# Kernel tuning notes

Measured on AMD Instinct MI355X. Metric: run time of the kernel, lower is better.

The kernel has to match this reference:

```python
import jax, jax.numpy as jnp
import numpy as np

EMBED_DIM = 1024
NUM_HEADS = 16
HEAD_DIM = EMBED_DIM // NUM_HEADS


def setup_inputs() -> dict:
    key = jax.random.key(0)
    ks = jax.random.split(key, 9)
    B, T, C = 2, 2048, EMBED_DIM
    s = 1.0 / np.sqrt(C)
    inp = {
        "x": jax.random.normal(ks[0], (B, T, C), dtype=jnp.float32),
        "Wq": jax.random.uniform(ks[1], (C, C), jnp.float32, -s, s),
        "bq": jax.random.uniform(ks[2], (C,), jnp.float32, -s, s),
        "Wk": jax.random.uniform(ks[3], (C, C), jnp.float32, -s, s),
        "bk": jax.random.uniform(ks[4], (C,), jnp.float32, -s, s),
        "Wv": jax.random.uniform(ks[5], (C, C), jnp.float32, -s, s),
        "bv": jax.random.uniform(ks[6], (C,), jnp.float32, -s, s),
        "Wo": jax.random.uniform(ks[7], (C, C), jnp.float32, -s, s),
        "bo": jax.random.uniform(ks[8], (C,), jnp.float32, -s, s),
    }
    return inp


def reference(x, Wq, bq, Wk, bk, Wv, bv, Wo, bo):
    B, T, C = x.shape
    H, D = NUM_HEADS, HEAD_DIM

    def heads(W, b):
        # [B,T,C] -> [B,H,T,D]
        return (x @ W + b).reshape(B, T, H, D).transpose(0, 2, 1, 3)

    q = heads(Wq, bq)
    k = heads(Wk, bk)
    v = heads(Wv, bv)

    scores = jnp.einsum('bhtd,bhsd->bhts', q, k) / np.sqrt(D).astype(np.float32)
    causal = jnp.tril(jnp.ones((T, T), dtype=bool))  # [T,T]
    scores = jnp.where(causal[None, None], scores, -jnp.inf)
    weights = jax.nn.softmax(scores, axis=-1)
    out = jnp.einsum('bhts,bhsd->bhtd', weights, v)  # [B,H,T,D]
    out = out.transpose(0, 2, 1, 3).reshape(B, T, C)
    return out @ Wo + bo
```

## Files before the change

### kernel.cpp

```cpp
#include <hip/hip_runtime.h>
#include <stdint.h>

#define T_LEN 2048
#define C_DIM 1024
#define NHEAD 16
#define HDIM  64
#define MTOT  4096

typedef __bf16 bf16;
typedef __bf16 bf16x8 __attribute__((ext_vector_type(8)));
typedef float  f32x4  __attribute__((ext_vector_type(4)));

__device__ __forceinline__ bf16 f2bf(float f) {
    union { float f; unsigned u; } x; x.f = f;
    unsigned r = x.u + 0x7fffu + ((x.u >> 16) & 1u);
    unsigned short h = (unsigned short)(r >> 16);
    return __builtin_bit_cast(bf16, h);
}

__device__ __forceinline__ void g2l16(const void* g, const void* l) {
    __builtin_amdgcn_global_load_lds(
        (const __attribute__((address_space(1))) unsigned int*)(uintptr_t)g,
        (__attribute__((address_space(3))) unsigned int*)(uint32_t)(uintptr_t)l,
        16, 0, 0);
}


__global__ void cast_x_kernel(const float* __restrict__ x, bf16* __restrict__ xb) {
    int f = blockIdx.x * 256 + threadIdx.x;
    const float4* p = (const float4*)x + (size_t)f * 2;
    float4 a = p[0], b = p[1];
    bf16x8 o;
    o[0] = f2bf(a.x); o[1] = f2bf(a.y); o[2] = f2bf(a.z); o[3] = f2bf(a.w);
    o[4] = f2bf(b.x); o[5] = f2bf(b.y); o[6] = f2bf(b.z); o[7] = f2bf(b.w);
    ((bf16x8*)xb)[f] = o;
}

__global__ void cast_w_kernel(const float* __restrict__ W0, const float* __restrict__ W1,
                              const float* __restrict__ W2, const float* __restrict__ W3,
                              bf16* __restrict__ wt) {
    __shared__ float tile[64][68];
    const int tid = threadIdx.x;
    const int w = blockIdx.z;
    const float* W = (w == 0) ? W0 : (w == 1) ? W1 : (w == 2) ? W2 : W3;
    const int kb = blockIdx.x * 64, nb = blockIdx.y * 64;
#pragma unroll
    for (int pass = 0; pass < 4; ++pass) {
        int row = pass * 16 + (tid >> 4);
        int col = (tid & 15) * 4;
        float4 v = *(const float4*)(W + (size_t)(kb + row) * 1024 + nb + col);
        *(float4*)(&tile[row][col]) = v;
    }
    __syncthreads();
#pragma unroll
    for (int pass = 0; pass < 2; ++pass) {
        int s = pass * 256 + tid;
        int nn = s >> 3, c = s & 7;
        bf16x8 o;
#pragma unroll
        for (int j = 0; j < 8; ++j) o[j] = f2bf(tile[c * 8 + j][nn]);
        *(bf16x8*)(wt + (size_t)w * 1048576 + (size_t)(nb + nn) * 1024 + kb + c * 8) = o;
    }
}

__global__ void transpose_v_kernel(const bf16* __restrict__ V, bf16* __restrict__ Vtp) {
    __shared__ bf16 tile[128][72];
    const int tid = threadIdx.x;
    const int t0 = blockIdx.x * 128, bh = blockIdx.y;
    const size_t hb = (size_t)bh * 131072;
#pragma unroll
    for (int pass = 0; pass < 4; ++pass) {
        int s = pass * 256 + tid;
        int row = s >> 3, c = s & 7;
        bf16x8 v = *(const bf16x8*)(V + hb + (size_t)(t0 + row) * 64 + c * 8);
        *(bf16x8*)(&tile[row][c * 8]) = v;
    }
    __syncthreads();
#pragma unroll
    for (int pass = 0; pass < 4; ++pass) {
        int s = pass * 256 + tid;
        int d = s >> 4, ch = s & 15;
        bf16x8 o;
#pragma unroll
        for (int j = 0; j < 8; ++j) o[j] = tile[j * 16 + ch][d];
        *(bf16x8*)(Vtp + hb + (size_t)d * 2048 + t0 + ch * 8) = o;
    }
}

__global__ __launch_bounds__(256, 3)
void gemm_bt_kernel(const bf16* __restrict__ A, const bf16* __restrict__ WtAll,
                    const float* __restrict__ b0, const float* __restrict__ b1,
                    const float* __restrict__ b2, bf16* __restrict__ outQKV) {
    __shared__ char lds[32768];
    bf16* As = (bf16*)lds;
    bf16* Bs = (bf16*)(lds + 16384);

    const int tid = threadIdx.x;
    const int lane = tid & 63, wid = tid >> 6;
    const int r = lane & 15, q4 = lane >> 4;
    const int mbase = blockIdx.y * 128;
    const int nbase = blockIdx.x * 128;
    const int z = blockIdx.z;
    const bf16* Bt = WtAll + (size_t)z * 1048576;
    const float* bias = (z == 0) ? b0 : (z == 1) ? b1 : b2;
    const float osc = (z == 0) ? 0.125f : 1.0f;

    const int wm = (wid >> 1) * 64;
    const int wn = (wid & 1) * 64;

    float bv[4];
#pragma unroll
    for (int j = 0; j < 4; ++j) bv[j] = bias[nbase + wn + j * 16 + r];

    f32x4 acc[4][4];
#pragma unroll
    for (int i = 0; i < 4; ++i)
#pragma unroll
        for (int j = 0; j < 4; ++j) acc[i][j] = f32x4{0.f, 0.f, 0.f, 0.f};

    for (int kt = 0; kt < 16; ++kt) {
        int kb = kt * 64;
#pragma unroll
        for (int p = 0; p < 4; ++p) {
            int s = p * 256 + tid;
            int row = s >> 3, blk = s & 7;
            int sb = blk ^ (row & 7);
            g2l16(A  + (size_t)(mbase + row) * 1024 + kb + sb * 8, (char*)As + s * 16);
            g2l16(Bt + (size_t)(nbase + row) * 1024 + kb + sb * 8, (char*)Bs + s * 16);
        }
        __syncthreads();
#pragma unroll
        for (int ks = 0; ks < 2; ++ks) {
            int blk = ks * 4 + q4;
            bf16x8 a[4], b[4];
#pragma unroll
            for (int i = 0; i < 4; ++i) {
                int rowa = wm + i * 16 + r;
                a[i] = *(const bf16x8*)((const char*)As + rowa * 128 + ((blk ^ (rowa & 7)) * 16));
                int rowb = wn + i * 16 + r;
                b[i] = *(const bf16x8*)((const char*)Bs + rowb * 128 + ((blk ^ (rowb & 7)) * 16));
            }
#pragma unroll
            for (int i = 0; i < 4; ++i)
#pragma unroll
                for (int j = 0; j < 4; ++j)
                    acc[i][j] = __builtin_amdgcn_mfma_f32_16x16x32_bf16(a[i], b[j], acc[i][j], 0, 0, 0);
        }
        __syncthreads();
    }

#pragma unroll
    for (int i = 0; i < 4; ++i) {
        int m0 = mbase + wm + i * 16 + q4 * 4;
#pragma unroll
        for (int j = 0; j < 4; ++j) {
            int n = nbase + wn + j * 16 + r;
#pragma unroll
            for (int reg = 0; reg < 4; ++reg) {
                float v = (acc[i][j][reg] + bv[j]) * osc;
                int mm = m0 + reg;
                int bi = mm >> 11, t = mm & 2047, h = n >> 6, d = n & 63;
                outQKV[(size_t)z * 4194304 + ((size_t)(bi * 16 + h) * 2048 + t) * 64 + d] = f2bf(v);
            }
        }
    }
}

__global__ __launch_bounds__(256, 2)
void gemm_o_kernel(const bf16* __restrict__ A, const bf16* __restrict__ Bt,
                   const float* __restrict__ bias, float* __restrict__ out) {
    __shared__ char lds[24576];
    bf16* As = (bf16*)lds;
    bf16* Bs = (bf16*)(lds + 16384);

    const int tid = threadIdx.x;
    const int lane = tid & 63, wid = tid >> 6;
    const int r = lane & 15, q4 = lane >> 4;
    const int nb = blockIdx.x * 64;
    const int mb = blockIdx.y * 128;
    const int wm = (wid >> 1) * 64;
    const int wn = (wid & 1) * 32;

    float bv[2];
#pragma unroll
    for (int j = 0; j < 2; ++j) bv[j] = bias[nb + wn + j * 16 + r];

    f32x4 acc[4][2];
#pragma unroll
    for (int i = 0; i < 4; ++i)
#pragma unroll
        for (int j = 0; j < 2; ++j) acc[i][j] = f32x4{0.f, 0.f, 0.f, 0.f};

    for (int kt = 0; kt < 16; ++kt) {
        int kb = kt * 64;
#pragma unroll
        for (int p = 0; p < 4; ++p) {
            int s = p * 256 + tid;
            int row = s >> 3, blk = s & 7;
            g2l16(A + (size_t)(mb + row) * 1024 + kb + ((blk ^ (row & 7)) * 8), (char*)As + s * 16);
        }
#pragma unroll
        for (int p = 0; p < 2; ++p) {
            int s = p * 256 + tid;
            int row = s >> 3, blk = s & 7;
            g2l16(Bt + (size_t)(nb + row) * 1024 + kb + ((blk ^ (row & 7)) * 8), (char*)Bs + s * 16);
        }
        __syncthreads();
#pragma unroll
        for (int ks = 0; ks < 2; ++ks) {
            int blk = ks * 4 + q4;
            bf16x8 a[4], b[2];
#pragma unroll
            for (int i = 0; i < 4; ++i) {
                int rowa = wm + i * 16 + r;
                a[i] = *(const bf16x8*)((const char*)As + rowa * 128 + ((blk ^ (rowa & 7)) * 16));
            }
#pragma unroll
            for (int j = 0; j < 2; ++j) {
                int rowb = wn + j * 16 + r;
                b[j] = *(const bf16x8*)((const char*)Bs + rowb * 128 + ((blk ^ (rowb & 7)) * 16));
            }
#pragma unroll
            for (int i = 0; i < 4; ++i)
#pragma unroll
                for (int j = 0; j < 2; ++j)
                    acc[i][j] = __builtin_amdgcn_mfma_f32_16x16x32_bf16(a[i], b[j], acc[i][j], 0, 0, 0);
        }
        __syncthreads();
    }

#pragma unroll
    for (int i = 0; i < 4; ++i) {
        int m0 = mb + wm + i * 16 + q4 * 4;
#pragma unroll
        for (int j = 0; j < 2; ++j) {
            int n = nb + wn + j * 16 + r;
#pragma unroll
            for (int reg = 0; reg < 4; ++reg)
                out[(size_t)(m0 + reg) * 1024 + n] = acc[i][j][reg] + bv[j];
        }
    }
}

__global__ __launch_bounds__(256, 1)
void attn_kernel(const bf16* __restrict__ Q, const bf16* __restrict__ K,
                 const bf16* __restrict__ Vtp, bf16* __restrict__ Aout) {
    __shared__ char lds[98304];

    const int tid = threadIdx.x, lane = tid & 63, wid = tid >> 6;
    const int r = lane & 15, q4 = lane >> 4;
    const int p = blockIdx.x >> 5;
    const int bh = blockIdx.x & 31;
    const int b = bh >> 4, h = bh & 15;
    const size_t hb = (size_t)bh * 131072;
    char* Pw = lds + 65536 + wid * 8192;

    const int qiA = p, qiB = 15 - p;
    const int itB0 = qiA + 1;
    const int ittot = itB0 + qiB + 1;

    bf16x8 qfA[2][2], qfB[2][2], qf[2][2];
#pragma unroll
    for (int i = 0; i < 2; ++i)
#pragma unroll
        for (int ks = 0; ks < 2; ++ks) {
            int rA = qiA * 128 + wid * 32 + i * 16 + r;
            int rB = qiB * 128 + wid * 32 + i * 16 + r;
            qfA[i][ks] = *(const bf16x8*)(Q + hb + (size_t)rA * 64 + ks * 32 + q4 * 8);
            qfB[i][ks] = *(const bf16x8*)(Q + hb + (size_t)rB * 64 + ks * 32 + q4 * 8);
            qf[i][ks] = qfA[i][ks];
        }

    f32x4 o[2][4];
    float lip[2][4];
#pragma unroll
    for (int i = 0; i < 2; ++i)
#pragma unroll
        for (int jd = 0; jd < 4; ++jd) { o[i][jd] = f32x4{0.f, 0.f, 0.f, 0.f}; lip[i][jd] = 0.f; }

    auto stage = [&](int buf, int kb) {
        char* Kb = lds + buf * 16384;
        char* Vb = lds + 32768 + buf * 16384;
#pragma unroll
        for (int pp = 0; pp < 4; ++pp) {
            int s = pp * 256 + tid;
            int row = s >> 3, blk = s & 7;
            g2l16(K + hb + (size_t)(kb + row) * 64 + ((blk ^ (row & 7)) * 8), Kb + s * 16);
        }
#pragma unroll
        for (int pp = 0; pp < 4; ++pp) {
            int s = pp * 256 + tid;
            int row = s >> 4, ch = s & 15;
            g2l16(Vtp + hb + (size_t)row * 2048 + kb + ((ch ^ (row & 15)) * 8), Vb + s * 16);
        }
    };

    auto epilogue = [&](int qbase) {
#pragma unroll
        for (int i = 0; i < 2; ++i)
#pragma unroll
            for (int reg = 0; reg < 4; ++reg) {
                float li = lip[i][reg];
                li += __shfl_xor(li, 1);
                li += __shfl_xor(li, 2);
                li += __shfl_xor(li, 4);
                li += __shfl_xor(li, 8);
                float inv = 1.f / li;
                int grow = qbase + wid * 32 + i * 16 + q4 * 4 + reg;
#pragma unroll
                for (int jd = 0; jd < 4; ++jd) {
                    int d = jd * 16 + r;
                    Aout[((size_t)(b * 2048 + grow)) * 1024 + h * 64 + d] = f2bf(o[i][jd][reg] * inv);
                }
            }
    };

    stage(0, 0);

    for (int it = 0; it < ittot; ++it) {
        __syncthreads();
        const int cb = it & 1;
        if (it + 1 < ittot) {
            int nit = it + 1;
            int nkt = (nit < itB0) ? nit : (nit - itB0);
            stage(nit & 1, nkt * 128);
        }
        if (it == itB0) {
            epilogue(qiA * 128);
#pragma unroll
            for (int i = 0; i < 2; ++i) {
#pragma unroll
                for (int jd = 0; jd < 4; ++jd) { o[i][jd] = f32x4{0.f, 0.f, 0.f, 0.f}; lip[i][jd] = 0.f; }
#pragma unroll
                for (int ks = 0; ks < 2; ++ks) qf[i][ks] = qfB[i][ks];
            }
        }
        const bool inB = (it >= itB0);
        const int qi = inB ? qiB : qiA;
        const int kt = inB ? (it - itB0) : it;
        const int kb = kt * 128;
        const int qbase = qi * 128;
        const char* Kb = lds + cb * 16384;
        const char* Vb = lds + 32768 + cb * 16384;

        f32x4 sc[2][8];
#pragma unroll
        for (int jn = 0; jn < 8; ++jn) {
            int rowk = jn * 16 + r;
            bf16x8 bk0 = *(const bf16x8*)(Kb + rowk * 128 + ((q4 ^ (rowk & 7)) * 16));
            bf16x8 bk1 = *(const bf16x8*)(Kb + rowk * 128 + (((4 + q4) ^ (rowk & 7)) * 16));
#pragma unroll
            for (int i = 0; i < 2; ++i) {
                sc[i][jn] = __builtin_amdgcn_mfma_f32_16x16x32_bf16(qf[i][0], bk0, f32x4{0.f, 0.f, 0.f, 0.f}, 0, 0, 0);
                sc[i][jn] = __builtin_amdgcn_mfma_f32_16x16x32_bf16(qf[i][1], bk1, sc[i][jn], 0, 0, 0);
            }
        }

        const bool lastt = (kt == qi);
#pragma unroll
        for (int i = 0; i < 2; ++i) {
#pragma unroll
            for (int reg = 0; reg < 4; ++reg) {
                int rowl = i * 16 + q4 * 4 + reg;
                int grow = qbase + wid * 32 + rowl;
                bf16x8 pp8;
                float rs = 0.f;
                if (lastt) {
#pragma unroll
                    for (int jn = 0; jn < 8; ++jn) {
                        float sv = (kb + jn * 16 + r > grow) ? -1e30f : sc[i][jn][reg];
                        float pv = __expf(sv);
                        rs += pv;
                        pp8[jn] = (bf16)pv;
                    }
                } else {
#pragma unroll
                    for (int jn = 0; jn < 8; ++jn) {
                        float pv = __expf(sc[i][jn][reg]);
                        rs += pv;
                        pp8[jn] = (bf16)pv;
                    }
                }
                lip[i][reg] += rs;
                *(bf16x8*)(Pw + rowl * 256 + ((r ^ (rowl & 15)) * 16)) = pp8;
            }
        }

#pragma unroll
        for (int s4 = 0; s4 < 4; ++s4) {
            int c = s4 * 4 + q4;
            bf16x8 ap0 = *(const bf16x8*)(Pw + r * 256 + ((c ^ r) * 16));
            bf16x8 ap1 = *(const bf16x8*)(Pw + (16 + r) * 256 + ((c ^ r) * 16));
#pragma unroll
            for (int jd = 0; jd < 4; ++jd) {
                int rowd = jd * 16 + r;
                bf16x8 bv8 = *(const bf16x8*)(Vb + rowd * 256 + ((c ^ (rowd & 15)) * 16));
                o[0][jd] = __builtin_amdgcn_mfma_f32_16x16x32_bf16(ap0, bv8, o[0][jd], 0, 0, 0);
                o[1][jd] = __builtin_amdgcn_mfma_f32_16x16x32_bf16(ap1, bv8, o[1][jd], 0, 0, 0);
            }
        }
    }

    epilogue(qiB * 128);
}


extern "C" void kernel_launch(void* const* d_in, const int* in_sizes, int n_in,
                              void* d_out, int out_size, void* d_ws, size_t ws_size,
                              hipStream_t stream) {
    const float* x  = (const float*)d_in[0];
    const float* Wq = (const float*)d_in[1];
    const float* bq = (const float*)d_in[2];
    const float* Wk = (const float*)d_in[3];
    const float* bk = (const float*)d_in[4];
    const float* Wv = (const float*)d_in[5];
    const float* bv = (const float*)d_in[6];
    const float* Wo = (const float*)d_in[7];
    const float* bo = (const float*)d_in[8];
    float* out = (float*)d_out;

    char* ws = (char*)d_ws;
    bf16* xb   = (bf16*)(ws);
    bf16* wt   = (bf16*)(ws + 8388608);
    bf16* qkv  = (bf16*)(ws + 16777216);
    bf16* vtp  = (bf16*)(ws + 41943040);
    bf16* attn = (bf16*)(ws + 50331648);

    hipLaunchKernelGGL(cast_x_kernel, dim3(2048), dim3(256), 0, stream, x, xb);
    hipLaunchKernelGGL(cast_w_kernel, dim3(16, 16, 4), dim3(256), 0, stream, Wq, Wk, Wv, Wo, wt);
    hipLaunchKernelGGL(gemm_bt_kernel, dim3(8, 32, 3), dim3(256), 0, stream,
                       xb, wt, bq, bk, bv, qkv);
    hipLaunchKernelGGL(transpose_v_kernel, dim3(16, 32), dim3(256), 0, stream,
                       qkv + (size_t)2 * 4194304, vtp);
    hipLaunchKernelGGL(attn_kernel, dim3(256), dim3(256), 0, stream,
                       qkv, qkv + 4194304, vtp, attn);
    hipLaunchKernelGGL(gemm_o_kernel, dim3(16, 32), dim3(256), 0, stream,
                       attn, wt + (size_t)3 * 1048576, bo, out);
}
```

Measured before the change: 184.9 us.

## Keep attention probabilities in registers via transposed MFMA and permuted V layout

```diff
diff --git a/kernel.cpp b/kernel.cpp
--- a/kernel.cpp
+++ b/kernel.cpp
@@ -8,6 +8,7 @@
 #define MTOT  4096
 
 typedef __bf16 bf16;
+typedef __bf16 bf16x4 __attribute__((ext_vector_type(4)));
 typedef __bf16 bf16x8 __attribute__((ext_vector_type(8)));
 typedef float  f32x4  __attribute__((ext_vector_type(4)));
 
@@ -82,12 +83,15 @@
         int d = s >> 4, ch = s & 15;
         bf16x8 o;
 #pragma unroll
-        for (int j = 0; j < 8; ++j) o[j] = tile[j * 16 + ch][d];
+        for (int j = 0; j < 8; ++j) {
+            int orig = 32 * (ch >> 2) + 16 * (j >> 2) + 4 * (ch & 3) + (j & 3);
+            o[j] = tile[orig][d];
+        }
         *(bf16x8*)(Vtp + hb + (size_t)d * 2048 + t0 + ch * 8) = o;
     }
 }
 
-__global__ __launch_bounds__(256, 3)
+__global__ __launch_bounds__(256, 2)
 void gemm_bt_kernel(const bf16* __restrict__ A, const bf16* __restrict__ WtAll,
                     const float* __restrict__ b0, const float* __restrict__ b1,
                     const float* __restrict__ b2, bf16* __restrict__ outQKV) {
@@ -245,7 +249,7 @@
 __global__ __launch_bounds__(256, 1)
 void attn_kernel(const bf16* __restrict__ Q, const bf16* __restrict__ K,
                  const bf16* __restrict__ Vtp, bf16* __restrict__ Aout) {
-    __shared__ char lds[98304];
+    __shared__ char lds[65536];
 
     const int tid = threadIdx.x, lane = tid & 63, wid = tid >> 6;
     const int r = lane & 15, q4 = lane >> 4;
@@ -253,30 +257,30 @@
     const int bh = blockIdx.x & 31;
     const int b = bh >> 4, h = bh & 15;
     const size_t hb = (size_t)bh * 131072;
-    char* Pw = lds + 65536 + wid * 8192;
 
     const int qiA = p, qiB = 15 - p;
     const int itB0 = qiA + 1;
     const int ittot = itB0 + qiB + 1;
 
-    bf16x8 qfA[2][2], qfB[2][2], qf[2][2];
+    bf16x8 qf[2][2], qfB[2][2];
 #pragma unroll
     for (int i = 0; i < 2; ++i)
 #pragma unroll
         for (int ks = 0; ks < 2; ++ks) {
             int rA = qiA * 128 + wid * 32 + i * 16 + r;
             int rB = qiB * 128 + wid * 32 + i * 16 + r;
-            qfA[i][ks] = *(const bf16x8*)(Q + hb + (size_t)rA * 64 + ks * 32 + q4 * 8);
+            qf[i][ks]  = *(const bf16x8*)(Q + hb + (size_t)rA * 64 + ks * 32 + q4 * 8);
             qfB[i][ks] = *(const bf16x8*)(Q + hb + (size_t)rB * 64 + ks * 32 + q4 * 8);
-            qf[i][ks] = qfA[i][ks];
         }
 
     f32x4 o[2][4];
-    float lip[2][4];
-#pragma unroll
-    for (int i = 0; i < 2; ++i)
-#pragma unroll
-        for (int jd = 0; jd < 4; ++jd) { o[i][jd] = f32x4{0.f, 0.f, 0.f, 0.f}; lip[i][jd] = 0.f; }
+    float lip[2];
+#pragma unroll
+    for (int i = 0; i < 2; ++i) {
+        lip[i] = 0.f;
+#pragma unroll
+        for (int jd = 0; jd < 4; ++jd) o[i][jd] = f32x4{0.f, 0.f, 0.f, 0.f};
+    }
 
     auto stage = [&](int buf, int kb) {
         char* Kb = lds + buf * 16384;
@@ -297,22 +301,20 @@
 
     auto epilogue = [&](int qbase) {
 #pragma unroll
-        for (int i = 0; i < 2; ++i)
-#pragma unroll
-            for (int reg = 0; reg < 4; ++reg) {
-                float li = lip[i][reg];
-                li += __shfl_xor(li, 1);
-                li += __shfl_xor(li, 2);
-                li += __shfl_xor(li, 4);
-                li += __shfl_xor(li, 8);
-                float inv = 1.f / li;
-                int grow = qbase + wid * 32 + i * 16 + q4 * 4 + reg;
-#pragma unroll
-                for (int jd = 0; jd < 4; ++jd) {
-                    int d = jd * 16 + r;
-                    Aout[((size_t)(b * 2048 + grow)) * 1024 + h * 64 + d] = f2bf(o[i][jd][reg] * inv);
-                }
-            }
+        for (int i = 0; i < 2; ++i) {
+            float li = lip[i];
+            li += __shfl_xor(li, 16);
+            li += __shfl_xor(li, 32);
+            float inv = 1.f / li;
+            int q = qbase + wid * 32 + i * 16 + r;
+#pragma unroll
+            for (int dsub = 0; dsub < 4; ++dsub) {
+                bf16x4 w;
+#pragma unroll
+                for (int reg = 0; reg < 4; ++reg) w[reg] = f2bf(o[i][dsub][reg] * inv);
+                *(bf16x4*)(Aout + ((size_t)(b * 2048 + q)) * 1024 + h * 64 + dsub * 16 + q4 * 4) = w;
+            }
+        }
     };
 
     stage(0, 0);
@@ -329,8 +331,9 @@
             epilogue(qiA * 128);
 #pragma unroll
             for (int i = 0; i < 2; ++i) {
-#pragma unroll
-                for (int jd = 0; jd < 4; ++jd) { o[i][jd] = f32x4{0.f, 0.f, 0.f, 0.f}; lip[i][jd] = 0.f; }
+                lip[i] = 0.f;
+#pragma unroll
+                for (int jd = 0; jd < 4; ++jd) o[i][jd] = f32x4{0.f, 0.f, 0.f, 0.f};
 #pragma unroll
                 for (int ks = 0; ks < 2; ++ks) qf[i][ks] = qfB[i][ks];
             }
@@ -345,58 +348,57 @@
 
         f32x4 sc[2][8];
 #pragma unroll
-        for (int jn = 0; jn < 8; ++jn) {
-            int rowk = jn * 16 + r;
-            bf16x8 bk0 = *(const bf16x8*)(Kb + rowk * 128 + ((q4 ^ (rowk & 7)) * 16));
-            bf16x8 bk1 = *(const bf16x8*)(Kb + rowk * 128 + (((4 + q4) ^ (rowk & 7)) * 16));
+        for (int st = 0; st < 8; ++st) {
+            int rowk = st * 16 + r;
+            bf16x8 ak0 = *(const bf16x8*)(Kb + rowk * 128 + ((q4 ^ (rowk & 7)) * 16));
+            bf16x8 ak1 = *(const bf16x8*)(Kb + rowk * 128 + (((4 + q4) ^ (rowk & 7)) * 16));
 #pragma unroll
             for (int i = 0; i < 2; ++i) {
-                sc[i][jn] = __builtin_amdgcn_mfma_f32_16x16x32_bf16(qf[i][0], bk0, f32x4{0.f, 0.f, 0.f, 0.f}, 0, 0, 0);
-                sc[i][jn] = __builtin_amdgcn_mfma_f32_16x16x32_bf16(qf[i][1], bk1, sc[i][jn], 0, 0, 0);
+                sc[i][st] = __builtin_amdgcn_mfma_f32_16x16x32_bf16(ak0, qf[i][0], f32x4{0.f, 0.f, 0.f, 0.f}, 0, 0, 0);
+                sc[i][st] = __builtin_amdgcn_mfma_f32_16x16x32_bf16(ak1, qf[i][1], sc[i][st], 0, 0, 0);
             }
         }
 
         const bool lastt = (kt == qi);
+        bf16x8 pb[2][4];
 #pragma unroll
         for (int i = 0; i < 2; ++i) {
-#pragma unroll
-            for (int reg = 0; reg < 4; ++reg) {
-                int rowl = i * 16 + q4 * 4 + reg;
-                int grow = qbase + wid * 32 + rowl;
-                bf16x8 pp8;
-                float rs = 0.f;
+            int qrow = qbase + wid * 32 + i * 16 + r;
+#pragma unroll
+            for (int c = 0; c < 4; ++c) {
+                bf16x8 t;
                 if (lastt) {
 #pragma unroll
-                    for (int jn = 0; jn < 8; ++jn) {
-                        float sv = (kb + jn * 16 + r > grow) ? -1e30f : sc[i][jn][reg];
+                    for (int j = 0; j < 8; ++j) {
+                        int st = 2 * c + (j >> 2), reg = j & 3;
+                        int key = kb + st * 16 + q4 * 4 + reg;
+                        float sv = (key > qrow) ? -1e30f : sc[i][st][reg];
                         float pv = __expf(sv);
-                        rs += pv;
-                        pp8[jn] = (bf16)pv;
+                        lip[i] += pv;
+                        t[j] = (bf16)pv;
                     }
                 } else {
 #pragma unroll
-                    for (int jn = 0; jn < 8; ++jn) {
-                        float pv = __expf(sc[i][jn][reg]);
-                        rs += pv;
-                        pp8[jn] = (bf16)pv;
+                    for (int j = 0; j < 8; ++j) {
+                        int st = 2 * c + (j >> 2), reg = j & 3;
+                        float pv = __expf(sc[i][st][reg]);
+                        lip[i] += pv;
+                        t[j] = (bf16)pv;
                     }
                 }
-                lip[i][reg] += rs;
-                *(bf16x8*)(Pw + rowl * 256 + ((r ^ (rowl & 15)) * 16)) = pp8;
-            }
-        }
-
-#pragma unroll
-        for (int s4 = 0; s4 < 4; ++s4) {
-            int c = s4 * 4 + q4;
-            bf16x8 ap0 = *(const bf16x8*)(Pw + r * 256 + ((c ^ r) * 16));
-            bf16x8 ap1 = *(const bf16x8*)(Pw + (16 + r) * 256 + ((c ^ r) * 16));
-#pragma unroll
-            for (int jd = 0; jd < 4; ++jd) {
-                int rowd = jd * 16 + r;
-                bf16x8 bv8 = *(const bf16x8*)(Vb + rowd * 256 + ((c ^ (rowd & 15)) * 16));
-                o[0][jd] = __builtin_amdgcn_mfma_f32_16x16x32_bf16(ap0, bv8, o[0][jd], 0, 0, 0);
-                o[1][jd] = __builtin_amdgcn_mfma_f32_16x16x32_bf16(ap1, bv8, o[1][jd], 0, 0, 0);
+                pb[i][c] = t;
+            }
+        }
+
+#pragma unroll
+        for (int c = 0; c < 4; ++c) {
+            int sidx = c * 4 + q4;
+#pragma unroll
+            for (int dsub = 0; dsub < 4; ++dsub) {
+                int rowd = dsub * 16 + r;
+                bf16x8 av = *(const bf16x8*)(Vb + rowd * 256 + ((sidx ^ (rowd & 15)) * 16));
+                o[0][dsub] = __builtin_amdgcn_mfma_f32_16x16x32_bf16(av, pb[0][c], o[0][dsub], 0, 0, 0);
+                o[1][dsub] = __builtin_amdgcn_mfma_f32_16x16x32_bf16(av, pb[1][c], o[1][dsub], 0, 0, 0);
             }
         }
     }
```

Measured after the change: 180.9 us. -2.1%, faster.
